# Kernel optimization log

Hardware: AMD Instinct MI355X
Metric: run time of the kernel (lower is better)

Reference implementation:

```python
import jax, jax.numpy as jnp
import numpy as np

B, S, HID, H = 2, 2048, 1024, 16
D = HID // H
ROTARY_BASE = 10000.0
LN_EPS = 1e-5
NEG = -1e9


def setup_inputs() -> dict:
    key = jax.random.key(0)
    ks = jax.random.split(key, 20)
    w = lambda k, shape: (jax.random.normal(k, shape, jnp.float32) * 0.02)
    return {
        "x": jax.random.normal(ks[0], (B, S, HID), jnp.float32),
        "mask": jnp.ones((B, S), jnp.int32),
        "wq": w(ks[1], (HID, HID)), "bq": jnp.zeros((HID,), jnp.float32),
        "wk": w(ks[2], (HID, HID)), "bk": jnp.zeros((HID,), jnp.float32),
        "wv": w(ks[3], (HID, HID)), "bv": jnp.zeros((HID,), jnp.float32),
        "wo": w(ks[4], (HID, HID)), "bo": jnp.zeros((HID,), jnp.float32),
        "w1": w(ks[5], (HID, 4 * HID)), "b1": jnp.zeros((4 * HID,), jnp.float32),
        "w2": w(ks[6], (4 * HID, HID)), "b2": jnp.zeros((HID,), jnp.float32),
        "ln1_g": jnp.ones((HID,), jnp.float32), "ln1_b": jnp.zeros((HID,), jnp.float32),
        "ln2_g": jnp.ones((HID,), jnp.float32), "ln2_b": jnp.zeros((HID,), jnp.float32),
    }


def _layer_norm(z, g, b):
    m = z.mean(-1, keepdims=True)
    v = ((z - m) ** 2).mean(-1, keepdims=True)
    return (z - m) / jnp.sqrt(v + LN_EPS) * g + b


def _rope(t, cos, sin):
    # t: [B,H,S,D]; even/odd halves rotated then CONCATENATED (matches source, not interleaved)
    e, o = t[..., 0::2], t[..., 1::2]
    return jnp.concatenate([e * cos - o * sin, e * sin + o * cos], axis=-1)


def reference(x, mask, wq, bq, wk, bk, wv, bv, wo, bo, w1, b1, w2, b2,
              ln1_g, ln1_b, ln2_g, ln2_b):
    b, s, hid = x.shape
    h, d = H, D
    # rotary tables for positions [0, s)
    inv_freq = 1.0 / (ROTARY_BASE ** (jnp.arange(0, d, 2, dtype=jnp.float32) / d))
    freqs = jnp.arange(s, dtype=jnp.float32)[:, None] * inv_freq[None, :]  # [S, D/2]
    cos = jnp.cos(freqs)[None, None]  # [1,1,S,D/2]
    sin = jnp.sin(freqs)[None, None]

    # ---- attention sublayer (pre-norm) ----
    xn = _layer_norm(x, ln1_g, ln1_b)
    q = (xn @ wq + bq).reshape(b, s, h, d).transpose(0, 2, 1, 3)
    k = (xn @ wk + bk).reshape(b, s, h, d).transpose(0, 2, 1, 3)
    v = (xn @ wv + bv).reshape(b, s, h, d).transpose(0, 2, 1, 3)
    q = _rope(q, cos, sin)
    k = _rope(k, cos, sin)

    scores = jnp.einsum('bhqd,bhkd->bhqk', q, k) / np.sqrt(d).astype(np.float32)
    pad = (mask == 0)[:, None, None, :]              # [B,1,1,S]
    scores = jnp.where(pad, NEG, scores)
    causal = jnp.triu(jnp.ones((s, s), bool), 1)     # [S,S]
    scores = jnp.where(causal, NEG, scores)
    probs = jax.nn.softmax(scores, axis=-1)          # dropout p=0.0 (eval)
    ctx = jnp.einsum('bhqk,bhkd->bhqd', probs, v)
    ctx = ctx.transpose(0, 2, 1, 3).reshape(b, s, hid)
    attn_out = ctx @ wo + bo
    x = x + attn_out

    # ---- FFN sublayer (pre-norm) ----
    xn = _layer_norm(x, ln2_g, ln2_b)
    f = jax.nn.gelu(xn @ w1 + b1, approximate=True) @ w2 + b2
    return x + f
```

## Files before the change

### kernel.cpp

```cpp
#include <hip/hip_runtime.h>

typedef unsigned short u16;
typedef unsigned int u32;
typedef __attribute__((ext_vector_type(8))) u16 u16x8;
typedef __attribute__((ext_vector_type(4))) u16 u16x4;
typedef __attribute__((ext_vector_type(8))) __bf16 bf16x8;
typedef __attribute__((ext_vector_type(4))) float f32x4;

static __device__ __forceinline__ float bf2f(u16 u) {
    union { u32 i; float f; } v; v.i = ((u32)u) << 16; return v.f;
}
static __device__ __forceinline__ u16 f2bf(float f) {
    union { float f; u32 i; } v; v.f = f;
    u32 r = v.i + 0x7fffu + ((v.i >> 16) & 1u);
    return (u16)(r >> 16);
}
static __device__ __forceinline__ u16 f2bfn(float f) {
    __bf16 h = (__bf16)f;
    return *(u16*)&h;
}
static __device__ __forceinline__ void gl_lds16(const void* gsrc, void* ldst) {
    __builtin_amdgcn_global_load_lds((const __attribute__((address_space(1))) void*)gsrc,
                                     (__attribute__((address_space(3))) void*)ldst, 16, 0, 0);
}

__global__ __launch_bounds__(256) void transpose_cvt4(const float* __restrict__ w0, const float* __restrict__ w1,
                                                      const float* __restrict__ w2, const float* __restrict__ w3,
                                                      u16* __restrict__ o0, u16* __restrict__ o1,
                                                      u16* __restrict__ o2, u16* __restrict__ o3) {
    __shared__ float t[32][33];
    const float* in; u16* out;
    switch (blockIdx.z) {
        case 0:  in = w0; out = o0; break;
        case 1:  in = w1; out = o1; break;
        case 2:  in = w2; out = o2; break;
        default: in = w3; out = o3; break;
    }
    int k0 = blockIdx.y << 5, n0 = blockIdx.x << 5;
    int r = threadIdx.x >> 3, c4 = threadIdx.x & 7;
    float4 v = *(const float4*)(in + (size_t)(k0 + r) * 1024 + n0 + (c4 << 2));
    t[r][c4 * 4 + 0] = v.x; t[r][c4 * 4 + 1] = v.y;
    t[r][c4 * 4 + 2] = v.z; t[r][c4 * 4 + 3] = v.w;
    __syncthreads();
    u16x4 o;
    o[0] = f2bf(t[c4 * 4 + 0][r]); o[1] = f2bf(t[c4 * 4 + 1][r]);
    o[2] = f2bf(t[c4 * 4 + 2][r]); o[3] = f2bf(t[c4 * 4 + 3][r]);
    *(u16x4*)(out + (size_t)(n0 + r) * 1024 + k0 + (c4 << 2)) = o;
}

__global__ __launch_bounds__(256) void transpose_cvt2(const float* __restrict__ w1, const float* __restrict__ w2,
                                                      u16* __restrict__ o1, u16* __restrict__ o2) {
    __shared__ float t[32][33];
    const int zz = blockIdx.z;
    const float* in = zz ? w2 : w1;
    u16* out = zz ? o2 : o1;
    const int K = zz ? 4096 : 1024, N = zz ? 1024 : 4096;
    int k0, n0;
    if (zz) { k0 = blockIdx.x << 5; n0 = blockIdx.y << 5; }
    else    { n0 = blockIdx.x << 5; k0 = blockIdx.y << 5; }
    int r = threadIdx.x >> 3, c4 = threadIdx.x & 7;
    float4 v = *(const float4*)(in + (size_t)(k0 + r) * N + n0 + (c4 << 2));
    t[r][c4 * 4 + 0] = v.x; t[r][c4 * 4 + 1] = v.y;
    t[r][c4 * 4 + 2] = v.z; t[r][c4 * 4 + 3] = v.w;
    __syncthreads();
    u16x4 o;
    o[0] = f2bf(t[c4 * 4 + 0][r]); o[1] = f2bf(t[c4 * 4 + 1][r]);
    o[2] = f2bf(t[c4 * 4 + 2][r]); o[3] = f2bf(t[c4 * 4 + 3][r]);
    *(u16x4*)(out + (size_t)(n0 + r) * K + k0 + (c4 << 2)) = o;
}

__global__ void prep_kernel(const float* __restrict__ bq, const float* __restrict__ bk,
                            const float* __restrict__ bv, float* __restrict__ bqkv,
                            const int* __restrict__ mask, float* __restrict__ maskf,
                            float* __restrict__ cost, float* __restrict__ sint) {
    int idx = blockIdx.x * 256 + threadIdx.x;
    int s = idx >> 5, f = idx & 31;
    float inv = powf(10000.0f, -((float)(2 * f)) / 64.0f);
    float a = (float)s * inv;
    cost[idx] = cosf(a);
    sint[idx] = sinf(a);
    if (idx < 3072) {
        float v = (idx < 1024) ? bq[idx] : (idx < 2048 ? bk[idx - 1024] : bv[idx - 2048]);
        bqkv[idx] = v;
    }
    if (idx < 4096) maskf[idx] = (float)mask[idx];
}

__global__ __launch_bounds__(256) void ln_kernel(const float* __restrict__ x,
                                                 const float* __restrict__ gam,
                                                 const float* __restrict__ bet,
                                                 u16* __restrict__ out) {
    int row = blockIdx.x, tid = threadIdx.x;
    float4 v = *((const float4*)(x + (size_t)row * 1024) + tid);
    float s = v.x + v.y + v.z + v.w;
    float sq = v.x * v.x + v.y * v.y + v.z * v.z + v.w * v.w;
    #pragma unroll
    for (int off = 32; off >= 1; off >>= 1) {
        s += __shfl_xor(s, off);
        sq += __shfl_xor(sq, off);
    }
    __shared__ float red[8];
    int wid = tid >> 6, lane = tid & 63;
    if (lane == 0) { red[wid] = s; red[wid + 4] = sq; }
    __syncthreads();
    float ts = red[0] + red[1] + red[2] + red[3];
    float tq = red[4] + red[5] + red[6] + red[7];
    float mean = ts * (1.0f / 1024.0f);
    float var = tq * (1.0f / 1024.0f) - mean * mean;
    float rstd = rsqrtf(var + 1e-5f);
    float4 g = ((const float4*)gam)[tid];
    float4 b = ((const float4*)bet)[tid];
    u16x4 o;
    o[0] = f2bfn((v.x - mean) * rstd * g.x + b.x);
    o[1] = f2bfn((v.y - mean) * rstd * g.y + b.y);
    o[2] = f2bfn((v.z - mean) * rstd * g.z + b.z);
    o[3] = f2bfn((v.w - mean) * rstd * g.w + b.w);
    *(u16x4*)(out + (size_t)row * 1024 + (tid << 2)) = o;
}

__global__ __launch_bounds__(256) void ln_fuse(float* __restrict__ x2, const u16* __restrict__ part,
                                               const float* __restrict__ gam, const float* __restrict__ bet,
                                               u16* __restrict__ out) {
    int row = blockIdx.x, tid = threadIdx.x;
    float4 v = *((const float4*)(x2 + (size_t)row * 1024) + tid);
    u16x4 pv = *(const u16x4*)(part + (size_t)row * 1024 + (tid << 2));
    v.x += bf2f(pv[0]); v.y += bf2f(pv[1]); v.z += bf2f(pv[2]); v.w += bf2f(pv[3]);
    *((float4*)(x2 + (size_t)row * 1024) + tid) = v;
    float s = v.x + v.y + v.z + v.w;
    float sq = v.x * v.x + v.y * v.y + v.z * v.z + v.w * v.w;
    #pragma unroll
    for (int off = 32; off >= 1; off >>= 1) {
        s += __shfl_xor(s, off);
        sq += __shfl_xor(sq, off);
    }
    __shared__ float red[8];
    int wid = tid >> 6, lane = tid & 63;
    if (lane == 0) { red[wid] = s; red[wid + 4] = sq; }
    __syncthreads();
    float ts = red[0] + red[1] + red[2] + red[3];
    float tq = red[4] + red[5] + red[6] + red[7];
    float mean = ts * (1.0f / 1024.0f);
    float var = tq * (1.0f / 1024.0f) - mean * mean;
    float rstd = rsqrtf(var + 1e-5f);
    float4 g = ((const float4*)gam)[tid];
    float4 b = ((const float4*)bet)[tid];
    u16x4 o;
    o[0] = f2bfn((v.x - mean) * rstd * g.x + b.x);
    o[1] = f2bfn((v.y - mean) * rstd * g.y + b.y);
    o[2] = f2bfn((v.z - mean) * rstd * g.z + b.z);
    o[3] = f2bfn((v.w - mean) * rstd * g.w + b.w);
    *(u16x4*)(out + (size_t)row * 1024 + (tid << 2)) = o;
}

template <int EPI>
__global__ __launch_bounds__(512, 2) void gemm256(const u16* __restrict__ A, const u16* __restrict__ Bt,
                                                  const float* __restrict__ bias,
                                                  u16* __restrict__ outb, int M, int N, int K) {
    __shared__ __align__(16) u16 lds[65536];
    const int tid = threadIdx.x;
    const int lane = tid & 63, wid = tid >> 6;
    const int cl = lane & 15, g4 = lane >> 4;
    const int wr = wid >> 2, wc = wid & 3;
    const int gx = gridDim.x;
    const int lid = blockIdx.y * gx + blockIdx.x;
    const int per8 = (gx * gridDim.y) >> 3;
    const int newlin = (lid & 7) * per8 + (lid >> 3);
    const int m0 = (newlin / gx) << 8;
    const int n0 = (newlin % gx) << 8;
    const int NT = K >> 6;
    f32x4 acc[8][4] = {};
    const int r0 = tid >> 3;          const int gc0 = (tid & 7) ^ (r0 & 7);
    const int r1 = (tid + 512) >> 3;  const int gc1 = (tid & 7) ^ (r1 & 7);
    const int wub = wid << 10;

    auto stageHalf = [&](int buf, int mat, int h, int kt) {
        const u16* src = mat ? Bt : A;
        const int base0 = mat ? n0 : m0;
        char* d = (char*)lds + buf * 65536 + mat * 32768 + h * 16384 + wub;
        gl_lds16(src + (size_t)(base0 + h * 128 + r0) * K + (kt << 6) + (gc0 << 3), d);
        gl_lds16(src + (size_t)(base0 + h * 128 + r1) * K + (kt << 6) + (gc1 << 3), d + 8192);
    };

    stageHalf(0, 0, 0, 0); stageHalf(0, 0, 1, 0);
    stageHalf(0, 1, 0, 0); stageHalf(0, 1, 1, 0);
    asm volatile("s_waitcnt vmcnt(0)" ::: "memory");
    __builtin_amdgcn_s_barrier();

    for (int t = 0; t < NT; ++t) {
        const int buf = t & 1, nbuf = buf ^ 1;
        const bool more = (t + 1 < NT);
        const int abase = buf * 65536 + wr * 16384;
        const int bbase = buf * 65536 + 32768 + (wc >> 1) * 16384;
        bf16x8 bfr[4][2];
        #pragma unroll
        for (int q = 0; q < 4; ++q) {
            bf16x8 afr[2][2];
            #pragma unroll
            for (int di = 0; di < 2; ++di)
                #pragma unroll
                for (int ks = 0; ks < 2; ++ks) {
                    int row = q * 32 + di * 16 + cl;
                    int gr = ks * 4 + g4;
                    afr[di][ks] = *(const bf16x8*)((char*)lds + abase + (((row << 3) + (gr ^ (row & 7))) << 4));
                }
            if (q == 0) {
                #pragma unroll
                for (int j = 0; j < 4; ++j)
                    #pragma unroll
                    for (int ks = 0; ks < 2; ++ks) {
                        int row = ((wc & 1) << 6) + j * 16 + cl;
                        int gr = ks * 4 + g4;
                        bfr[j][ks] = *(const bf16x8*)((char*)lds + bbase + (((row << 3) + (gr ^ (row & 7))) << 4));
                    }
            }
            if (more) stageHalf(nbuf, q >> 1, q & 1, t + 1);
            __builtin_amdgcn_s_barrier();
            asm volatile("s_waitcnt lgkmcnt(0)" ::: "memory");
            __builtin_amdgcn_sched_barrier(0);
            __builtin_amdgcn_s_setprio(1);
            #pragma unroll
            for (int di = 0; di < 2; ++di)
                #pragma unroll
                for (int j = 0; j < 4; ++j)
                    #pragma unroll
                    for (int ks = 0; ks < 2; ++ks)
                        acc[q * 2 + di][j] = __builtin_amdgcn_mfma_f32_16x16x32_bf16(
                            afr[di][ks], bfr[j][ks], acc[q * 2 + di][j], 0, 0, 0);
            __builtin_amdgcn_s_setprio(0);
            if (q == 3 && more) asm volatile("s_waitcnt vmcnt(0)" ::: "memory");
            __builtin_amdgcn_s_barrier();
            if (q == 3) __builtin_amdgcn_sched_barrier(0);
        }
    }
    #pragma unroll
    for (int i = 0; i < 8; ++i)
        #pragma unroll
        for (int j = 0; j < 4; ++j) {
            int row = m0 + wr * 128 + i * 16 + g4 * 4;
            int col = n0 + wc * 64 + j * 16 + cl;
            float bc = bias[col];
            #pragma unroll
            for (int rr = 0; rr < 4; ++rr) {
                float v = acc[i][j][rr] + bc;
                size_t idx = (size_t)(row + rr) * N + col;
                if constexpr (EPI == 0) {
                    outb[idx] = f2bfn(v);
                } else {
                    float tg = 0.7978845608f * (v + 0.044715f * v * v * v);
                    outb[idx] = f2bfn(v / (1.0f + exp2f(tg * -2.88539008f)));
                }
            }
        }
}

__global__ __launch_bounds__(512, 2) void gemm256r(const u16* __restrict__ A, const u16* __restrict__ Bt,
                                                   const float* __restrict__ bias,
                                                   const float* __restrict__ res,
                                                   float* __restrict__ outf, u16* __restrict__ poutb,
                                                   int M, int N, int K) {
    __shared__ __align__(16) u16 lds[65536];
    const int tid = threadIdx.x;
    const int lane = tid & 63, wid = tid >> 6;
    const int cl = lane & 15, g4 = lane >> 4;
    const int wr = wid >> 2, wc = wid & 3;
    const int gx = gridDim.x;
    const int lid = blockIdx.y * gx + blockIdx.x;
    const int per8 = (gx * gridDim.y) >> 3;
    const int newlin = (lid & 7) * per8 + (lid >> 3);
    const int m0 = (newlin / gx) << 8;
    const int n0 = (newlin % gx) << 8;
    const int kchunk = K / gridDim.z;
    const int kbase = blockIdx.z * kchunk;
    const int NT = kchunk >> 6;
    f32x4 acc[8][4] = {};
    const int r0 = tid >> 3;          const int gc0 = (tid & 7) ^ (r0 & 7);
    const int r1 = (tid + 512) >> 3;  const int gc1 = (tid & 7) ^ (r1 & 7);
    const int wub = wid << 10;

    auto stageHalf = [&](int buf, int mat, int h, int kt) {
        const u16* src = mat ? Bt : A;
        const int base0 = mat ? n0 : m0;
        char* d = (char*)lds + buf * 65536 + mat * 32768 + h * 16384 + wub;
        gl_lds16(src + (size_t)(base0 + h * 128 + r0) * K + kbase + (kt << 6) + (gc0 << 3), d);
        gl_lds16(src + (size_t)(base0 + h * 128 + r1) * K + kbase + (kt << 6) + (gc1 << 3), d + 8192);
    };

    stageHalf(0, 0, 0, 0); stageHalf(0, 0, 1, 0);
    stageHalf(0, 1, 0, 0); stageHalf(0, 1, 1, 0);
    asm volatile("s_waitcnt vmcnt(0)" ::: "memory");
    __builtin_amdgcn_s_barrier();

    for (int t = 0; t < NT; ++t) {
        const int buf = t & 1, nbuf = buf ^ 1;
        const bool more = (t + 1 < NT);
        const int abase = buf * 65536 + wr * 16384;
        const int bbase = buf * 65536 + 32768 + (wc >> 1) * 16384;
        bf16x8 bfr[4][2];
        #pragma unroll
        for (int q = 0; q < 4; ++q) {
            bf16x8 afr[2][2];
            #pragma unroll
            for (int di = 0; di < 2; ++di)
                #pragma unroll
                for (int ks = 0; ks < 2; ++ks) {
                    int row = q * 32 + di * 16 + cl;
                    int gr = ks * 4 + g4;
                    afr[di][ks] = *(const bf16x8*)((char*)lds + abase + (((row << 3) + (gr ^ (row & 7))) << 4));
                }
            if (q == 0) {
                #pragma unroll
                for (int j = 0; j < 4; ++j)
                    #pragma unroll
                    for (int ks = 0; ks < 2; ++ks) {
                        int row = ((wc & 1) << 6) + j * 16 + cl;
                        int gr = ks * 4 + g4;
                        bfr[j][ks] = *(const bf16x8*)((char*)lds + bbase + (((row << 3) + (gr ^ (row & 7))) << 4));
                    }
            }
            if (more) stageHalf(nbuf, q >> 1, q & 1, t + 1);
            __builtin_amdgcn_s_barrier();
            asm volatile("s_waitcnt lgkmcnt(0)" ::: "memory");
            __builtin_amdgcn_sched_barrier(0);
            __builtin_amdgcn_s_setprio(1);
            #pragma unroll
            for (int di = 0; di < 2; ++di)
                #pragma unroll
                for (int j = 0; j < 4; ++j)
                    #pragma unroll
                    for (int ks = 0; ks < 2; ++ks)
                        acc[q * 2 + di][j] = __builtin_amdgcn_mfma_f32_16x16x32_bf16(
                            afr[di][ks], bfr[j][ks], acc[q * 2 + di][j], 0, 0, 0);
            __builtin_amdgcn_s_setprio(0);
            if (q == 3 && more) asm volatile("s_waitcnt vmcnt(0)" ::: "memory");
            __builtin_amdgcn_s_barrier();
            if (q == 3) __builtin_amdgcn_sched_barrier(0);
        }
    }
    if (blockIdx.z == 0) {
        #pragma unroll
        for (int i = 0; i < 8; ++i)
            #pragma unroll
            for (int j = 0; j < 4; ++j) {
                int row = m0 + wr * 128 + i * 16 + g4 * 4;
                int col = n0 + wc * 64 + j * 16 + cl;
                float bc = bias[col];
                #pragma unroll
                for (int rr = 0; rr < 4; ++rr) {
                    size_t idx = (size_t)(row + rr) * N + col;
                    outf[idx] = acc[i][j][rr] + bc + res[idx];
                }
            }
    } else {
        const size_t pbase = (size_t)(blockIdx.z - 1) * ((size_t)M * N);
        #pragma unroll
        for (int i = 0; i < 8; ++i)
            #pragma unroll
            for (int j = 0; j < 4; ++j) {
                int row = m0 + wr * 128 + i * 16 + g4 * 4;
                int col = n0 + wc * 64 + j * 16 + cl;
                #pragma unroll
                for (int rr = 0; rr < 4; ++rr)
                    poutb[pbase + (size_t)(row + rr) * N + col] = f2bfn(acc[i][j][rr]);
            }
    }
}

template <int EPI>
__global__ __launch_bounds__(256) void gemm_bt(const u16* __restrict__ A, const u16* __restrict__ Bt,
                                               const float* __restrict__ bias,
                                               const float* __restrict__ res,
                                               u16* __restrict__ outb, float* __restrict__ outf,
                                               u16* __restrict__ poutb,
                                               int M, int N, int K) {
    __shared__ __align__(16) u16 As[3][4096];
    __shared__ __align__(16) u16 Bs[3][4096];
    const int tid = threadIdx.x;
    const int lane = tid & 63, wid = tid >> 6;
    const int g = lane >> 4, cl = lane & 15;
    const int wr = wid >> 1, wc = wid & 1;
    const int gx = gridDim.x;
    const int lid = blockIdx.y * gx + blockIdx.x;
    const int per8 = (gx * gridDim.y) >> 3;
    const int newlin = (lid & 7) * per8 + (lid >> 3);
    const int m0 = (newlin / gx) << 7;
    const int n0 = (newlin % gx) << 7;
    const int kchunk = K / gridDim.z;
    const int kbase = blockIdx.z * kchunk;
    const int NT = kchunk >> 5;
    f32x4 acc[4][4] = {};
    const int grow = tid >> 2;
    const int gcol = (tid & 3) ^ ((tid >> 3) & 3);

    auto stage = [&](int buf, int kt) {
        const int ko = kbase + (kt << 5);
        gl_lds16(A + (size_t)(m0 + grow) * K + ko + (gcol << 3),       &As[buf][wid << 9]);
        gl_lds16(A + (size_t)(m0 + grow + 64) * K + ko + (gcol << 3),  &As[buf][(wid << 9) + 2048]);
        gl_lds16(Bt + (size_t)(n0 + grow) * K + ko + (gcol << 3),      &Bs[buf][wid << 9]);
        gl_lds16(Bt + (size_t)(n0 + grow + 64) * K + ko + (gcol << 3), &Bs[buf][(wid << 9) + 2048]);
    };

    stage(0, 0);
    stage(1, 1);
    for (int kt = 0; kt < NT; ++kt) {
        if (kt + 1 < NT) asm volatile("s_waitcnt vmcnt(4)" ::: "memory");
        else             asm volatile("s_waitcnt vmcnt(0)" ::: "memory");
        __builtin_amdgcn_s_barrier();
        __builtin_amdgcn_sched_barrier(0);
        if (kt + 2 < NT) stage((kt + 2) % 3, kt + 2);
        const int cb = kt % 3;
        bf16x8 a[4], b[4];
        #pragma unroll
        for (int i = 0; i < 4; ++i) {
            int row = (wr << 6) + (i << 4) + cl;
            a[i] = *(const bf16x8*)&As[cb][((row << 2) + (g ^ ((row >> 1) & 3))) << 3];
        }
        #pragma unroll
        for (int j = 0; j < 4; ++j) {
            int row = (wc << 6) + (j << 4) + cl;
            b[j] = *(const bf16x8*)&Bs[cb][((row << 2) + (g ^ ((row >> 1) & 3))) << 3];
        }
        __builtin_amdgcn_s_setprio(1);
        #pragma unroll
        for (int i = 0; i < 4; ++i)
            #pragma unroll
            for (int j = 0; j < 4; ++j)
                acc[i][j] = __builtin_amdgcn_mfma_f32_16x16x32_bf16(a[i], b[j], acc[i][j], 0, 0, 0);
        __builtin_amdgcn_s_setprio(0);
    }
    if (blockIdx.z == 0) {
        #pragma unroll
        for (int i = 0; i < 4; ++i)
            #pragma unroll
            for (int j = 0; j < 4; ++j) {
                int row = m0 + (wr << 6) + (i << 4) + (g << 2);
                int col = n0 + (wc << 6) + (j << 4) + cl;
                float bc = bias[col];
                #pragma unroll
                for (int rr = 0; rr < 4; ++rr) {
                    float v = acc[i][j][rr] + bc;
                    size_t idx = (size_t)(row + rr) * N + col;
                    outf[idx] = v + res[idx];
                }
            }
    } else {
        const size_t pbase = (size_t)(blockIdx.z - 1) * ((size_t)M * N);
        #pragma unroll
        for (int i = 0; i < 4; ++i)
            #pragma unroll
            for (int j = 0; j < 4; ++j) {
                int row = m0 + (wr << 6) + (i << 4) + (g << 2);
                int col = n0 + (wc << 6) + (j << 4) + cl;
                #pragma unroll
                for (int rr = 0; rr < 4; ++rr)
                    poutb[pbase + (size_t)(row + rr) * N + col] = f2bfn(acc[i][j][rr]);
            }
    }
}

__global__ __launch_bounds__(256) void reduce_addb(float* __restrict__ out, const u16* __restrict__ p,
                                                   int nparts) {
    int i = blockIdx.x * 256 + threadIdx.x;
    float4 a = ((const float4*)out)[i];
    for (int j = 0; j < nparts; ++j) {
        u16x4 v = *(const u16x4*)(p + (size_t)j * 4194304 + ((size_t)i << 2));
        a.x += bf2f(v[0]); a.y += bf2f(v[1]); a.z += bf2f(v[2]); a.w += bf2f(v[3]);
    }
    ((float4*)out)[i] = a;
}

__global__ __launch_bounds__(256) void rope_qk(const u16* __restrict__ qkv,
                                               const float* __restrict__ cost,
                                               const float* __restrict__ sint,
                                               u16* __restrict__ qr, u16* __restrict__ kr) {
    int tid = threadIdx.x;
    int rowid = (blockIdx.x << 4) + (tid >> 4);
    int j = tid & 15;
    int half = j >> 3, jj = j & 7;
    int b = rowid >> 15;
    int h = (rowid >> 11) & 15;
    int s = rowid & 2047;
    size_t qbase = (size_t)((b << 11) + s) * 3072 + (h << 6);
    float cf[4], sf_[4];
    {
        float4 c = *(const float4*)(cost + (s << 5) + (jj << 2));
        float4 sn = *(const float4*)(sint + (s << 5) + (jj << 2));
        cf[0] = c.x; cf[1] = c.y; cf[2] = c.z; cf[3] = c.w;
        sf_[0] = sn.x; sf_[1] = sn.y; sf_[2] = sn.z; sf_[3] = sn.w;
    }
    size_t obase = (size_t)rowid * 64 + (half << 5) + (jj << 2);
    {
        u16x8 v = *(const u16x8*)(qkv + qbase + (jj << 3));
        u16x4 o;
        #pragma unroll
        for (int m2 = 0; m2 < 4; ++m2) {
            float e = bf2f(v[2 * m2]), od = bf2f(v[2 * m2 + 1]);
            float val = (half == 0) ? (e * cf[m2] - od * sf_[m2]) : (e * sf_[m2] + od * cf[m2]);
            o[m2] = f2bfn(val * 0.1803368801f);
        }
        *(u16x4*)(qr + obase) = o;
    }
    {
        u16x8 v = *(const u16x8*)(qkv + qbase + 1024 + (jj << 3));
        u16x4 o;
        #pragma unroll
        for (int m2 = 0; m2 < 4; ++m2) {
            float e = bf2f(v[2 * m2]), od = bf2f(v[2 * m2 + 1]);
            float val = (half == 0) ? (e * cf[m2] - od * sf_[m2]) : (e * sf_[m2] + od * cf[m2]);
            o[m2] = f2bfn(val);
        }
        *(u16x4*)(kr + obase) = o;
    }
}

__global__ __launch_bounds__(256) void v_transpose(const u16* __restrict__ qkv,
                                                   u16* __restrict__ vt) {
    __shared__ __align__(16) u16 tl[64 * 80];
    int stile = blockIdx.x, bh = blockIdx.y;
    int b = bh >> 4, h = bh & 15;
    int tid = threadIdx.x;
    #pragma unroll
    for (int i = 0; i < 2; ++i) {
        int slot = tid + (i << 8);
        int srow = slot >> 3, c = slot & 7;
        u16x8 v = *(const u16x8*)(qkv + (size_t)((b << 11) + (stile << 6) + srow) * 3072 + 2048 + (h << 6) + (c << 3));
        *(u16x8*)(tl + srow * 80 + (c << 3)) = v;
    }
    __syncthreads();
    #pragma unroll
    for (int i = 0; i < 2; ++i) {
        int slot = tid + (i << 8);
        int drow = slot >> 3, c = slot & 7;
        u16x8 o;
        #pragma unroll
        for (int m2 = 0; m2 < 8; ++m2) o[m2] = tl[(c * 8 + m2) * 80 + drow];
        *(u16x8*)(vt + ((size_t)bh * 64 + drow) * 2048 + (stile << 6) + (c << 3)) = o;
    }
}

__global__ __launch_bounds__(256) void attn_kernel(const u16* __restrict__ Q, const u16* __restrict__ Kd,
                                                   const u16* __restrict__ Vt, const float* __restrict__ maskf,
                                                   u16* __restrict__ ctx) {
    __shared__ __align__(16) u16 Ks[3][4096];
    __shared__ __align__(16) u16 Vs[3][4096];
    __shared__ __align__(16) u16 Ps[4096];
    const int tid = threadIdx.x, lane = tid & 63, w = tid >> 6;
    const int g = lane >> 4, cl = lane & 15;
    const int lid = blockIdx.y * 16 + blockIdx.x;
    const int xcd = lid & 7, slot = lid >> 3;
    const int bh = xcd * 4 + (slot >> 4);
    const int pair = slot & 15;
    const int b = bh >> 4, h = bh & 15;
    const u16* Kb = Kd + (size_t)bh * 2048 * 64;
    const u16* Vb = Vt + (size_t)bh * 64 * 2048;
    const int sr = tid >> 3;
    const int sg = (tid & 7) ^ (sr & 7);
    bf16x8 onesb;
    #pragma unroll
    for (int i2 = 0; i2 < 8; ++i2) onesb[i2] = (__bf16)1.0f;
    char* const pwb = (char*)Ps + w * 2048 + cl * 128 + ((g & 1) << 3);

    #pragma unroll
    for (int ci = 0; ci < 2; ++ci) {
        const int qb = (ci == 0) ? (31 - pair) : pair;
        const size_t qoff = ((size_t)bh * 2048 + qb * 64 + w * 16 + cl) * 64;
        const bf16x8 qa0 = *(const bf16x8*)(Q + qoff + (g << 3));
        const bf16x8 qa1 = *(const bf16x8*)(Q + qoff + 32 + (g << 3));
        const int qrow = qb * 64 + w * 16 + cl;
        f32x4 acc[4] = {};
        f32x4 lsum = {};

        auto stage = [&](int buf, int t) {
            char* kd = (char*)&Ks[buf][0] + (w << 10);
            char* vd = (char*)&Vs[buf][0] + (w << 10);
            const u16* Kg = Kb + (size_t)(t * 64) * 64;
            gl_lds16(Kg + (size_t)sr * 64 + (sg << 3), kd);
            gl_lds16(Kg + (size_t)(sr + 32) * 64 + (sg << 3), kd + 4096);
            gl_lds16(Vb + (size_t)sr * 2048 + t * 64 + (sg << 3), vd);
            gl_lds16(Vb + (size_t)(sr + 32) * 2048 + t * 64 + (sg << 3), vd + 4096);
        };

        __syncthreads();
        stage(0, 0);
        if (qb >= 1) {
            stage(1, 1);
            asm volatile("s_waitcnt vmcnt(4)" ::: "memory");
        } else {
            asm volatile("s_waitcnt vmcnt(0)" ::: "memory");
        }
        __syncthreads();

        for (int t = 0; t <= qb; ++t) {
            const bool more = (t < qb);
            if (t + 2 <= qb) stage((t + 2) % 3, t + 2);
            const int cur = t % 3;
            f32x4 sf[4];
            __builtin_amdgcn_s_setprio(1);
            #pragma unroll
            for (int ct = 0; ct < 4; ++ct) {
                f32x4 s = {};
                int krow = ct * 16 + cl;
                bf16x8 kb0 = *(const bf16x8*)((char*)&Ks[cur][0] + krow * 128 + ((g ^ (krow & 7)) << 4));
                bf16x8 kb1 = *(const bf16x8*)((char*)&Ks[cur][0] + krow * 128 + (((4 + g) ^ (krow & 7)) << 4));
                s = __builtin_amdgcn_mfma_f32_16x16x32_bf16(kb0, qa0, s, 0, 0, 0);
                s = __builtin_amdgcn_mfma_f32_16x16x32_bf16(kb1, qa1, s, 0, 0, 0);
                sf[ct] = s;
            }
            __builtin_amdgcn_s_setprio(0);
            const bool diag = (t == qb);
            #pragma unroll
            for (int ct = 0; ct < 4; ++ct) {
                const int kc0 = t * 64 + ct * 16 + (g << 2);
                const float4 mv = *(const float4*)(maskf + (b << 11) + kc0);
                float p0 = exp2f(sf[ct][0]) * mv.x;
                float p1 = exp2f(sf[ct][1]) * mv.y;
                float p2 = exp2f(sf[ct][2]) * mv.z;
                float p3 = exp2f(sf[ct][3]) * mv.w;
                if (diag) {
                    p0 = (kc0 + 0 <= qrow) ? p0 : 0.0f;
                    p1 = (kc0 + 1 <= qrow) ? p1 : 0.0f;
                    p2 = (kc0 + 2 <= qrow) ? p2 : 0.0f;
                    p3 = (kc0 + 3 <= qrow) ? p3 : 0.0f;
                }
                u32 lo, hi;
                asm("v_cvt_pk_bf16_f32 %0, %1, %2" : "=v"(lo) : "v"(p0), "v"(p1));
                asm("v_cvt_pk_bf16_f32 %0, %1, %2" : "=v"(hi) : "v"(p2), "v"(p3));
                uint2 pk; pk.x = lo; pk.y = hi;
                *(uint2*)(pwb + ((((ct << 1) + (g >> 1)) ^ (cl & 7)) << 4)) = pk;
            }
            __builtin_amdgcn_s_setprio(1);
            #pragma unroll
            for (int kc = 0; kc < 2; ++kc) {
                bf16x8 pa = *(const bf16x8*)((char*)Ps + w * 2048 + cl * 128 + (((kc * 4 + g) ^ (cl & 7)) << 4));
                lsum = __builtin_amdgcn_mfma_f32_16x16x32_bf16(pa, onesb, lsum, 0, 0, 0);
                #pragma unroll
                for (int n = 0; n < 4; ++n) {
                    int vrow = n * 16 + cl;
                    bf16x8 vb = *(const bf16x8*)((char*)&Vs[cur][0] + vrow * 128 + (((kc * 4 + g) ^ (vrow & 7)) << 4));
                    acc[n] = __builtin_amdgcn_mfma_f32_16x16x32_bf16(pa, vb, acc[n], 0, 0, 0);
                }
            }
            __builtin_amdgcn_s_setprio(0);
            if (more) {
                if (t + 2 <= qb) asm volatile("s_waitcnt vmcnt(4)" ::: "memory");
                else             asm volatile("s_waitcnt vmcnt(0)" ::: "memory");
                __syncthreads();
                __builtin_amdgcn_sched_barrier(0);
            }
        }
        #pragma unroll
        for (int n = 0; n < 4; ++n)
            #pragma unroll
            for (int rr = 0; rr < 4; ++rr) {
                int token = (b << 11) + qb * 64 + w * 16 + g * 4 + rr;
                int col = (h << 6) + n * 16 + cl;
                ctx[(size_t)token * 1024 + col] = f2bfn(acc[n][rr] / lsum[rr]);
            }
    }
}

extern "C" void kernel_launch(void* const* d_in, const int* in_sizes, int n_in,
                              void* d_out, int out_size, void* d_ws, size_t ws_size,
                              hipStream_t stream) {
    const float* x   = (const float*)d_in[0];
    const int* mask  = (const int*)d_in[1];
    const float* wq  = (const float*)d_in[2];
    const float* bq  = (const float*)d_in[3];
    const float* wk  = (const float*)d_in[4];
    const float* bk  = (const float*)d_in[5];
    const float* wv  = (const float*)d_in[6];
    const float* bv  = (const float*)d_in[7];
    const float* wo  = (const float*)d_in[8];
    const float* bo  = (const float*)d_in[9];
    const float* w1  = (const float*)d_in[10];
    const float* b1  = (const float*)d_in[11];
    const float* w2  = (const float*)d_in[12];
    const float* b2  = (const float*)d_in[13];
    const float* g1  = (const float*)d_in[14];
    const float* be1 = (const float*)d_in[15];
    const float* g2  = (const float*)d_in[16];
    const float* be2 = (const float*)d_in[17];
    float* out = (float*)d_out;
    char* ws = (char*)d_ws;

    u16* wqkvT  = (u16*)(ws + 0);
    u16* woT    = (u16*)(ws + 6291456);
    u16* w1T    = (u16*)(ws + 8388608);
    u16* w2T    = (u16*)(ws + 16777216);
    float* bqkv = (float*)(ws + 25165824);
    float* cost = (float*)(ws + 25178112);
    float* sint = (float*)(ws + 25440256);
    u16* xn     = (u16*)(ws + 25702400);
    float* x2   = (float*)(ws + 34091008);
    float* maskf= (float*)(ws + 34091008);
    u16* qkv    = (u16*)(ws + 50868224);
    u16* ffh    = (u16*)(ws + 50868224);
    u16* qr     = (u16*)(ws + 76034048);
    u16* kr     = (u16*)(ws + 84422656);
    u16* vt     = (u16*)(ws + 92811264);
    u16* ctx    = (u16*)(ws + 101199872);
    u16* partb  = (u16*)(ws + 84422656);

    transpose_cvt4<<<dim3(32, 32, 4), 256, 0, stream>>>(wq, wk, wv, wo,
                                                        wqkvT, wqkvT + 1024 * 1024, wqkvT + 2048 * 1024, woT);
    transpose_cvt2<<<dim3(128, 32, 2), 256, 0, stream>>>(w1, w2, w1T, w2T);
    prep_kernel<<<256, 256, 0, stream>>>(bq, bk, bv, bqkv, mask, maskf, cost, sint);

    ln_kernel<<<4096, 256, 0, stream>>>(x, g1, be1, xn);
    gemm256<0><<<dim3(12, 16), 512, 0, stream>>>(xn, wqkvT, bqkv, qkv, 4096, 3072, 1024);
    rope_qk<<<4096, 256, 0, stream>>>(qkv, cost, sint, qr, kr);
    v_transpose<<<dim3(32, 32), 256, 0, stream>>>(qkv, vt);
    attn_kernel<<<dim3(16, 32), 256, 0, stream>>>(qr, kr, vt, maskf, ctx);
    gemm_bt<1><<<dim3(8, 32, 2), 256, 0, stream>>>(ctx, woT, bo, x, nullptr, x2, partb, 4096, 1024, 1024);
    ln_fuse<<<4096, 256, 0, stream>>>(x2, partb, g2, be2, xn);
    gemm256<2><<<dim3(16, 16), 512, 0, stream>>>(xn, w1T, b1, ffh, 4096, 4096, 1024);
    gemm256r<<<dim3(4, 16, 4), 512, 0, stream>>>(ffh, w2T, b2, x2, out, partb, 4096, 1024, 4096);
    reduce_addb<<<4096, 256, 0, stream>>>(out, partb, 3);
}
```

Baseline: 246.1 us.

## Load K and V fragments directly from global memory in attention kernel

```diff
diff --git a/kernel.cpp b/kernel.cpp
--- a/kernel.cpp
+++ b/kernel.cpp
@@ -540,8 +540,6 @@
 __global__ __launch_bounds__(256) void attn_kernel(const u16* __restrict__ Q, const u16* __restrict__ Kd,
                                                    const u16* __restrict__ Vt, const float* __restrict__ maskf,
                                                    u16* __restrict__ ctx) {
-    __shared__ __align__(16) u16 Ks[3][4096];
-    __shared__ __align__(16) u16 Vs[3][4096];
     __shared__ __align__(16) u16 Ps[4096];
     const int tid = threadIdx.x, lane = tid & 63, w = tid >> 6;
     const int g = lane >> 4, cl = lane & 15;
@@ -552,12 +550,11 @@
     const int b = bh >> 4, h = bh & 15;
     const u16* Kb = Kd + (size_t)bh * 2048 * 64;
     const u16* Vb = Vt + (size_t)bh * 64 * 2048;
-    const int sr = tid >> 3;
-    const int sg = (tid & 7) ^ (sr & 7);
     bf16x8 onesb;
     #pragma unroll
     for (int i2 = 0; i2 < 8; ++i2) onesb[i2] = (__bf16)1.0f;
     char* const pwb = (char*)Ps + w * 2048 + cl * 128 + ((g & 1) << 3);
+    const u16* const vrow0 = Vb + (size_t)cl * 2048 + (g << 3);
 
     #pragma unroll
     for (int ci = 0; ci < 2; ++ci) {
@@ -569,40 +566,20 @@
         f32x4 acc[4] = {};
         f32x4 lsum = {};
 
-        auto stage = [&](int buf, int t) {
-            char* kd = (char*)&Ks[buf][0] + (w << 10);
-            char* vd = (char*)&Vs[buf][0] + (w << 10);
-            const u16* Kg = Kb + (size_t)(t * 64) * 64;
-            gl_lds16(Kg + (size_t)sr * 64 + (sg << 3), kd);
-            gl_lds16(Kg + (size_t)(sr + 32) * 64 + (sg << 3), kd + 4096);
-            gl_lds16(Vb + (size_t)sr * 2048 + t * 64 + (sg << 3), vd);
-            gl_lds16(Vb + (size_t)(sr + 32) * 2048 + t * 64 + (sg << 3), vd + 4096);
-        };
-
-        __syncthreads();
-        stage(0, 0);
-        if (qb >= 1) {
-            stage(1, 1);
-            asm volatile("s_waitcnt vmcnt(4)" ::: "memory");
-        } else {
-            asm volatile("s_waitcnt vmcnt(0)" ::: "memory");
-        }
-        __syncthreads();
-
         for (int t = 0; t <= qb; ++t) {
-            const bool more = (t < qb);
-            if (t + 2 <= qb) stage((t + 2) % 3, t + 2);
-            const int cur = t % 3;
+            bf16x8 kf[4][2];
+            #pragma unroll
+            for (int ct = 0; ct < 4; ++ct)
+                #pragma unroll
+                for (int ks = 0; ks < 2; ++ks)
+                    kf[ct][ks] = *(const bf16x8*)(Kb + ((size_t)(t * 64 + ct * 16 + cl)) * 64 + (((ks << 2) + g) << 3));
             f32x4 sf[4];
             __builtin_amdgcn_s_setprio(1);
             #pragma unroll
             for (int ct = 0; ct < 4; ++ct) {
                 f32x4 s = {};
-                int krow = ct * 16 + cl;
-                bf16x8 kb0 = *(const bf16x8*)((char*)&Ks[cur][0] + krow * 128 + ((g ^ (krow & 7)) << 4));
-                bf16x8 kb1 = *(const bf16x8*)((char*)&Ks[cur][0] + krow * 128 + (((4 + g) ^ (krow & 7)) << 4));
-                s = __builtin_amdgcn_mfma_f32_16x16x32_bf16(kb0, qa0, s, 0, 0, 0);
-                s = __builtin_amdgcn_mfma_f32_16x16x32_bf16(kb1, qa1, s, 0, 0, 0);
+                s = __builtin_amdgcn_mfma_f32_16x16x32_bf16(kf[ct][0], qa0, s, 0, 0, 0);
+                s = __builtin_amdgcn_mfma_f32_16x16x32_bf16(kf[ct][1], qa1, s, 0, 0, 0);
                 sf[ct] = s;
             }
             __builtin_amdgcn_s_setprio(0);
@@ -634,18 +611,11 @@
                 lsum = __builtin_amdgcn_mfma_f32_16x16x32_bf16(pa, onesb, lsum, 0, 0, 0);
                 #pragma unroll
                 for (int n = 0; n < 4; ++n) {
-                    int vrow = n * 16 + cl;
-                    bf16x8 vb = *(const bf16x8*)((char*)&Vs[cur][0] + vrow * 128 + (((kc * 4 + g) ^ (vrow & 7)) << 4));
+                    bf16x8 vb = *(const bf16x8*)(vrow0 + (size_t)(n << 4) * 2048 + t * 64 + (kc << 5));
                     acc[n] = __builtin_amdgcn_mfma_f32_16x16x32_bf16(pa, vb, acc[n], 0, 0, 0);
                 }
             }
             __builtin_amdgcn_s_setprio(0);
-            if (more) {
-                if (t + 2 <= qb) asm volatile("s_waitcnt vmcnt(4)" ::: "memory");
-                else             asm volatile("s_waitcnt vmcnt(0)" ::: "memory");
-                __syncthreads();
-                __builtin_amdgcn_sched_barrier(0);
-            }
         }
         #pragma unroll
         for (int n = 0; n < 4; ++n)
```

Result: slower. 323.0 us (+31.2%).
